# Optimization experiments

Hardware: AMD Instinct MI355X
Metric: run time of the kernel (lower is better)

Reference implementation:

```python
import jax, jax.numpy as jnp
import numpy as np

BETA = 0.25


def setup_inputs() -> dict:
    key = jax.random.key(0)
    k1, k2 = jax.random.split(key)
    z = jax.random.normal(k1, (16, 256, 32, 32), dtype=jnp.float32)
    # nn.Embedding init: uniform(-1/K, 1/K) with K = in_channels = 16384
    K, D = 16384, 256
    emb = jax.random.uniform(k2, (K, D), dtype=jnp.float32,
                             minval=-1.0 / K, maxval=1.0 / K)
    return {"z": z, "emb": emb}


def reference(z, emb):
    K, D = emb.shape
    # NCHW -> NHWC, flatten to tokens
    zp = jnp.transpose(z, (0, 2, 3, 1))            # [B,H,W,D]
    zf = zp.reshape(-1, D)                          # [N,D]
    # squared L2 distances: ||z||^2 + ||e||^2 - 2 z.e  -> [N,K]
    d = (jnp.sum(zf * zf, axis=1, keepdims=True)
         + jnp.sum(emb * emb, axis=1)
         - 2.0 * jnp.matmul(zf, emb.T))
    idx = jnp.argmin(d, axis=1)                     # [N] int
    # gather via direct lookup (equivalent to one-hot @ emb)
    z_q = emb[idx].reshape(zp.shape)                # [B,H,W,D]
    # commitment + codebook loss
    loss = (jnp.mean((jax.lax.stop_gradient(z_q) - zp) ** 2)
            + BETA * jnp.mean((z_q - jax.lax.stop_gradient(zp)) ** 2))
    # perplexity from code usage histogram (same as mean of one-hot rows)
    counts = jax.ops.segment_sum(jnp.ones_like(idx, dtype=jnp.float32), idx,
                                 num_segments=K)
    e_mean = counts / idx.shape[0]
    perplexity = jnp.exp(-jnp.sum(e_mean * jnp.log(e_mean + 1e-10)))
    # straight-through estimator, back to NCHW
    z_q_st = zp + jax.lax.stop_gradient(z_q - zp)
    z_q_out = jnp.transpose(z_q_st, (0, 3, 1, 2))   # [B,D,H,W]
    return z_q_out, loss, perplexity, idx
```

## Files before the change

kernel.cpp:

```cpp
#include <hip/hip_runtime.h>
#include <math.h>

#define NTOK   16384
#define DDIM   256
#define HWD    1024
#define CHW    262144
#define MARGIN 3.0e-4f
#define CLIPF  5.5f
#define QS     (127.0f/5.5f)
#define EQS    2080768.0f
#define SCALE  (5.5f/(127.0f*127.0f*16384.0f))

#define WS_TI8   0u
#define WS_CI8   4194304u
#define WS_M1    8388608u
#define WS_M2    16777216u
#define WS_ARG   25165824u
#define WS_FLG   29360128u
#define WS_EE    29376512u
#define WS_ZZ    29442048u
#define WS_IDX   29507584u
#define WS_CNT   29573120u
#define WS_SUM   29638656u

typedef __attribute__((ext_vector_type(4)))  int   i32x4;
typedef __attribute__((ext_vector_type(16))) char  c16;
typedef __attribute__((ext_vector_type(4)))  _Float16 h4;

__device__ __forceinline__ void top2m(int& a1, int& a2, const int b1, const int b2) {
  const int mn = min(a1, b1);
  a1 = max(a1, b1);
  a2 = max(max(a2, b2), mn);
}

__global__ __launch_bounds__(256) void k_prep(const float* __restrict__ z,
                                              const float* __restrict__ emb,
                                              char* __restrict__ Ti8,
                                              char* __restrict__ Ci8,
                                              float* __restrict__ zz,
                                              float* __restrict__ ee,
                                              float* __restrict__ zt,
                                              unsigned char* __restrict__ flags) {
  const int bid = blockIdx.x;
  const int tid = threadIdx.x;
  const int t64 = tid & 63, chunk = tid >> 6;
  if (bid < 256) {
    __shared__ double part[4][64];
    __shared__ int   fpart[4][64];
    const int n = bid * 64 + t64;
    const int b = n >> 10, hw = n & 1023;
    const float* zp = z + (size_t)b * CHW + hw;
    float tmp[64];
    double s = 0.0;
    int clip = 0;
    #pragma unroll
    for (int j = 0; j < 64; ++j) {
      const float f = zp[(size_t)(chunk * 64 + j) * HWD];
      tmp[j] = f;
      s += (double)f * (double)f;
      clip |= (fabsf(f) > CLIPF) ? 1 : 0;
    }
    c16 q[4];
    #pragma unroll
    for (int sl = 0; sl < 4; ++sl)
      #pragma unroll
      for (int j = 0; j < 16; ++j)
        q[sl][j] = (char)(int)rintf(fminf(fmaxf(tmp[sl * 16 + j], -CLIPF), CLIPF) * QS);
    const int rl = n & 127, tile = n >> 7;
    char* dst = Ti8 + (size_t)tile * 32768 + chunk * 8192 + rl * 64;
    const int sw = ((rl >> 1) & 3) << 4;
    #pragma unroll
    for (int sl = 0; sl < 4; ++sl) *(c16*)(dst + ((sl * 16) ^ sw)) = q[sl];
    float* ztp = zt + (size_t)n * 256 + chunk * 64;
    #pragma unroll
    for (int j4 = 0; j4 < 16; ++j4) *(float4*)(ztp + j4 * 4) = *(float4*)&tmp[j4 * 4];
    part[chunk][t64] = s;
    fpart[chunk][t64] = clip;
    __syncthreads();
    if (tid < 64) {
      zz[n] = (float)(part[0][t64] + part[1][t64] + part[2][t64] + part[3][t64]);
      flags[n] = (unsigned char)(fpart[0][t64] | fpart[1][t64] | fpart[2][t64] | fpart[3][t64]);
    }
  } else {
    __shared__ float rows[64][257];
    __shared__ double part2[4][64];
    const int k0 = (bid - 256) * 64;
    for (int i = tid; i < 16384; i += 256)
      rows[i >> 8][i & 255] = emb[(size_t)k0 * DDIM + i];
    __syncthreads();
    const int code = k0 + t64;
    double s = 0.0;
    c16 q[4];
    #pragma unroll
    for (int sl = 0; sl < 4; ++sl)
      #pragma unroll
      for (int j = 0; j < 16; ++j) {
        const float f = rows[t64][chunk * 64 + sl * 16 + j];
        q[sl][j] = (char)(int)rintf(f * EQS);
        s += (double)f * (double)f;
      }
    char* dst = Ci8 + (size_t)code * 256 + chunk * 64;
    #pragma unroll
    for (int sl = 0; sl < 4; ++sl) *(c16*)(dst + sl * 16) = q[sl];
    part2[chunk][t64] = s;
    __syncthreads();
    if (tid < 64)
      ee[code] = (float)(part2[0][t64] + part2[1][t64] + part2[2][t64] + part2[3][t64]);
  }
}

__global__ __launch_bounds__(256) void k_mdist(
    const char* __restrict__ tokimg, const char* __restrict__ codrows,
    _Float16* __restrict__ M1, _Float16* __restrict__ M2,
    unsigned char* __restrict__ ARG) {
  __shared__ __attribute__((aligned(16))) char ldsB[65536];
  __shared__ _Float16 m1l[256];
  __shared__ _Float16 m2l[256];
  __shared__ unsigned char agl[256];
  const int raw = blockIdx.x;
  const int p = raw & 7;
  const int ctile = p * 16 + ((raw >> 3) & 15);
  const int tgrp = raw >> 7;
  const int tid = threadIdx.x;
  const int w = tid >> 6, lane = tid & 63;
  const int wr = w >> 1, wc = w & 1;
  const int fr = lane & 15, fq = lane >> 4;

  i32x4 afr[4][4];
  {
    const char* ab = codrows + (size_t)(ctile * 128 + wr * 64 + fr) * 256 + fq * 16;
    #pragma unroll
    for (int m = 0; m < 4; ++m)
      #pragma unroll
      for (int kc = 0; kc < 4; ++kc)
        afr[m][kc] = *(const i32x4*)(ab + m * 16 * 256 + kc * 64);
  }

  int boff[4][4];
  #pragma unroll
  for (int n = 0; n < 4; ++n)
    #pragma unroll
    for (int kc = 0; kc < 4; ++kc) {
      const int t = wc * 64 + n * 16 + fr;
      boff[n][kc] = kc * 8192 + t * 64 + ((fq * 16) ^ (((t >> 1) & 3) << 4));
    }

  #define STAGEB(buf, tt)                                                             \
    {                                                                                 \
      const char* src = tokimg + (size_t)(tt) * 32768;                                \
      char* dstb = ldsB + (buf) * 32768;                                              \
      _Pragma("unroll")                                                               \
      for (int r = 0; r < 8; ++r) {                                                   \
        const int u = r * 256 + tid;                                                  \
        __builtin_amdgcn_global_load_lds(                                             \
            (const __attribute__((address_space(1))) void*)(src + u * 16),            \
            (__attribute__((address_space(3))) void*)(dstb + u * 16), 16, 0, 0);      \
      }                                                                               \
    }

  STAGEB(0, tgrp * 8);
  __syncthreads();

  const int fq4 = fq * 4;
  for (int it = 0; it < 8; ++it) {
    const int ttile = tgrp * 8 + it;
    if (it < 7) STAGEB((it + 1) & 1, ttile + 1);
    const char* bufb = ldsB + (it & 1) * 32768;

    i32x4 acc[4][4];
    #pragma unroll
    for (int m = 0; m < 4; ++m)
      #pragma unroll
      for (int n = 0; n < 4; ++n) acc[m][n] = (i32x4)0;

    #pragma unroll
    for (int kc = 0; kc < 4; ++kc) {
      i32x4 b[4];
      #pragma unroll
      for (int n = 0; n < 4; ++n) b[n] = *(const i32x4*)(bufb + boff[n][kc]);
      #pragma unroll
      for (int m = 0; m < 4; ++m)
        #pragma unroll
        for (int n = 0; n < 4; ++n)
          acc[m][n] = __builtin_amdgcn_mfma_i32_16x16x64_i8(afr[m][kc], b[n], acc[m][n], 0, 0, 0);
    }

    #pragma unroll
    for (int n = 0; n < 4; ++n) {
      int p1[8], p2[8];
      #pragma unroll
      for (int m = 0; m < 4; ++m)
        #pragma unroll
        for (int jj = 0; jj < 2; ++jj) {
          const int k0 = (acc[m][n][2 * jj]     << 8) | (m * 16 + fq4 + 2 * jj);
          const int k1 = (acc[m][n][2 * jj + 1] << 8) | (m * 16 + fq4 + 2 * jj + 1);
          p1[m * 2 + jj] = max(k0, k1);
          p2[m * 2 + jj] = min(k0, k1);
        }
      top2m(p1[0], p2[0], p1[1], p2[1]); top2m(p1[2], p2[2], p1[3], p2[3]);
      top2m(p1[4], p2[4], p1[5], p2[5]); top2m(p1[6], p2[6], p1[7], p2[7]);
      top2m(p1[0], p2[0], p1[2], p2[2]); top2m(p1[4], p2[4], p1[6], p2[6]);
      top2m(p1[0], p2[0], p1[4], p2[4]);
      int k1 = p1[0], k2 = p2[0];
      #pragma unroll
      for (int off = 16; off <= 32; off <<= 1) {
        const int o1 = __shfl_xor(k1, off, 64);
        const int o2 = __shfl_xor(k2, off, 64);
        top2m(k1, k2, o1, o2);
      }
      if (lane < 16) {
        const int tl = wc * 64 + n * 16 + fr;
        m1l[tl * 2 + wr] = (_Float16)(-2.0f * SCALE * (float)(k1 >> 8));
        m2l[tl * 2 + wr] = (_Float16)(-2.0f * SCALE * (float)(k2 >> 8));
        agl[tl * 2 + wr] = (unsigned char)(k1 & 255);
      }
    }
    __syncthreads();
    if (tid < 128) {
      const int tok = ttile * 128 + tid;
      *(unsigned int*)((char*)M1 + (size_t)tok * 512 + ctile * 4) =
          *(const unsigned int*)(m1l + tid * 2);
      M2[(size_t)(ctile * 2) * NTOK + tok]     = m2l[tid * 2];
      M2[(size_t)(ctile * 2 + 1) * NTOK + tok] = m2l[tid * 2 + 1];
      ARG[(size_t)(ctile * 2) * NTOK + tok]     = agl[tid * 2];
      ARG[(size_t)(ctile * 2 + 1) * NTOK + tok] = agl[tid * 2 + 1];
    }
    __syncthreads();
  }
}

__global__ __launch_bounds__(256) void k_pick(
    const float* __restrict__ zt, const float* __restrict__ emb,
    const float* __restrict__ zz, const float* __restrict__ ee,
    const _Float16* __restrict__ M1, const _Float16* __restrict__ M2,
    const unsigned char* __restrict__ ARG, const unsigned char* __restrict__ flags,
    int* __restrict__ idx, float* __restrict__ out_idxf) {
  __shared__ float zrow[4][260];
  __shared__ int   clist[4][576];
  __shared__ int   wcnt[4];
  const int tid = threadIdx.x;
  const int w = tid >> 6, lane = tid & 63;
  const int g16 = lane >> 4, l16 = lane & 15;
  for (int ni = 0; ni < 2; ++ni) {
    const int n = blockIdx.x * 8 + w * 2 + ni;
    if (lane == 0) wcnt[w] = 0;
    *(float4*)&zrow[w][lane * 4] = *(const float4*)(zt + (size_t)n * 256 + lane * 4);
    const h4 mv = *(const h4*)(M1 + (size_t)n * 256 + lane * 4);
    float ta4[4];
    #pragma unroll
    for (int s = 0; s < 4; ++s) ta4[s] = (float)mv[s];
    float mr = fminf(fminf(ta4[0], ta4[1]), fminf(ta4[2], ta4[3]));
    #pragma unroll
    for (int o = 32; o; o >>= 1) mr = fminf(mr, __shfl_xor(mr, o, 64));
    const int ex0 = flags[n];
    const float thr = ex0 ? 3.0e38f : mr + MARGIN;
    if (!ex0) {
      #pragma unroll
      for (int s = 0; s < 4; ++s) {
        if (ta4[s] <= thr) {
          const int sub = lane * 4 + s;
          const float m2v = (float)M2[(size_t)sub * NTOK + n];
          if (m2v > thr) {
            const int pos = atomicAdd(&wcnt[w], 1);
            if (pos < 576) clist[w][pos] = sub * 64 + (int)ARG[(size_t)sub * NTOK + n];
          } else {
            const int pos = atomicAdd(&wcnt[w], 64);
            if (pos + 64 <= 576)
              for (int i = 0; i < 64; ++i) clist[w][pos + i] = sub * 64 + i;
          }
        }
      }
    }
    const int cnt = wcnt[w];
    const int doEx = ex0 || (cnt > 576);
    const int nc = doEx ? 16384 : cnt;
    const float zzn = zz[n];
    unsigned long long best = ~0ull;
    for (int ci = 0; ci < nc; ci += 4) {
      int k;
      if (doEx) k = ci + g16;
      else { const int sl = ci + g16; k = clist[w][sl < cnt ? sl : 0]; }
      const float* erow = emb + (size_t)k * DDIM;
      double s = 0.0;
      #pragma unroll
      for (int qq = 0; qq < 4; ++qq) {
        const float4 ev = *(const float4*)(erow + qq * 64 + l16 * 4);
        const float4 zv = *(const float4*)(&zrow[w][qq * 64 + l16 * 4]);
        s += (double)zv.x * (double)ev.x + (double)zv.y * (double)ev.y
           + (double)zv.z * (double)ev.z + (double)zv.w * (double)ev.w;
      }
      #pragma unroll
      for (int o = 8; o; o >>= 1) s += __shfl_xor(s, o, 16);
      if (l16 == 0) {
        const float mm = (float)s;
        const float d = (zzn + ee[k]) - 2.0f * mm;
        const unsigned long long c =
            ((unsigned long long)__float_as_uint(d) << 32) | (unsigned int)k;
        if (c < best) best = c;
      }
    }
    unsigned long long b0 = (l16 == 0) ? best : ~0ull;
    {
      const unsigned long long o1 = __shfl_xor(b0, 16, 64);
      b0 = o1 < b0 ? o1 : b0;
      const unsigned long long o2 = __shfl_xor(b0, 32, 64);
      b0 = o2 < b0 ? o2 : b0;
    }
    if (lane == 0) {
      const int k0 = (int)(b0 & 0xffffffffu);
      idx[n] = k0;
      out_idxf[n] = (float)k0;
    }
  }
}

__global__ __launch_bounds__(256) void k_scatter(
    const float* __restrict__ z, const float* __restrict__ emb,
    const int* __restrict__ idx, float* __restrict__ out_zq,
    int* __restrict__ counts, double* __restrict__ sums) {
  __shared__ float et[64][257];
  __shared__ int sidx[64];
  __shared__ double w4[4];
  const int tg = blockIdx.x;
  const int n0 = tg * 64;
  const int b = n0 >> 10, hw0 = n0 & 1023;
  const int tid = threadIdx.x;
  if (tid < 64) sidx[tid] = idx[n0 + tid];
  __syncthreads();
  for (int i = tid; i < 16384; i += 256) {
    const int t = i >> 8, d = i & 255;
    et[t][d] = emb[(size_t)sidx[t] * DDIM + d];
  }
  __syncthreads();
  const float* zb = z + (size_t)b * CHW + hw0;
  float* ob = out_zq + (size_t)b * CHW + hw0;
  double s = 0.0;
  for (int i = tid; i < 16384; i += 256) {
    const int d = i >> 6, t = i & 63;
    const float v = et[t][d];
    const float diff = v - zb[(size_t)d * HWD + t];
    ob[(size_t)d * HWD + t] = v;
    s += (double)diff * (double)diff;
  }
  #pragma unroll
  for (int o = 32; o; o >>= 1) s += __shfl_xor(s, o, 64);
  const int wd = tid >> 6, lane = tid & 63;
  if (lane == 0) w4[wd] = s;
  __syncthreads();
  if (tid == 0) atomicAdd(&sums[0], w4[0] + w4[1] + w4[2] + w4[3]);
  if (tid < 64) atomicAdd(&counts[sidx[tid]], 1);
}

__global__ __launch_bounds__(256) void k_histfinal(const int* __restrict__ counts,
                                                   const double* __restrict__ sums,
                                                   float* __restrict__ out_loss,
                                                   float* __restrict__ out_perp) {
  __shared__ double w4[4];
  const int tid = threadIdx.x;
  double s = 0.0;
  for (int i = tid; i < 16384; i += 256) {
    const float em = (float)counts[i] * (1.0f / 16384.0f);
    s += (double)(em * logf(em + 1e-10f));
  }
  #pragma unroll
  for (int o = 32; o; o >>= 1) s += __shfl_xor(s, o, 64);
  const int wid = tid >> 6, lane = tid & 63;
  if (lane == 0) w4[wid] = s;
  __syncthreads();
  if (tid == 0) {
    const double S = w4[0] + w4[1] + w4[2] + w4[3];
    out_loss[0] = (float)(1.25 * sums[0] / 4194304.0);
    out_perp[0] = (float)exp(-S);
  }
}

extern "C" void kernel_launch(void* const* d_in, const int* in_sizes, int n_in,
                              void* d_out, int out_size, void* d_ws, size_t ws_size,
                              hipStream_t stream) {
  const float* z   = (const float*)d_in[0];
  const float* emb = (const float*)d_in[1];
  float* out      = (float*)d_out;
  float* out_zq   = out;
  float* out_loss = out + 4194304;
  float* out_perp = out + 4194305;
  float* out_idxf = out + 4194306;
  float* zt       = out;

  char* ws = (char*)d_ws;
  char* Ti8 = ws + WS_TI8;
  char* Ci8 = ws + WS_CI8;
  _Float16* M1 = (_Float16*)(ws + WS_M1);
  _Float16* M2 = (_Float16*)(ws + WS_M2);
  unsigned char* ARG = (unsigned char*)(ws + WS_ARG);
  unsigned char* flags = (unsigned char*)(ws + WS_FLG);
  float*  ee      = (float*)(ws + WS_EE);
  float*  zz      = (float*)(ws + WS_ZZ);
  int*    idx     = (int*)  (ws + WS_IDX);
  int*    counts  = (int*)  (ws + WS_CNT);
  double* sums    = (double*)(ws + WS_SUM);

  hipMemsetAsync(counts, 0, 65536 + 16, stream);

  k_prep <<<512, 256, 0, stream>>>(z, emb, Ti8, Ci8, zz, ee, zt, flags);
  k_mdist<<<2048, 256, 0, stream>>>(Ti8, Ci8, M1, M2, ARG);
  k_pick <<<2048, 256, 0, stream>>>(zt, emb, zz, ee, M1, M2, ARG, flags, idx, out_idxf);
  k_scatter<<<256, 256, 0, stream>>>(z, emb, idx, out_zq, counts, sums);
  k_histfinal<<<1, 256, 0, stream>>>(counts, sums, out_loss, out_perp);
}
```

Before: 207.7 us.

## Fuse loss and histogram into pick kernel, double-buffer mdist epilogue

Moves the code-usage histogram atomics and the squared-error loss accumulation into k_pick. The loss reuses the best distance already computed there, and per-block partial sums are reduced in k_histfinal. This lets k_scatter drop its strided reread of z and its atomics. In k_mdist the LDS epilogue staging is double-buffered to remove the trailing barrier, and MFMA issue priority is raised with s_setprio. The risk is that the loss now comes from the distance value rather than the exact (z_q - z)^2, which may shift precision.

```diff
diff --git a/kernel.cpp b/kernel.cpp
--- a/kernel.cpp
+++ b/kernel.cpp
@@ -21,7 +21,7 @@
 #define WS_ZZ    29442048u
 #define WS_IDX   29507584u
 #define WS_CNT   29573120u
-#define WS_SUM   29638656u
+#define WS_LSUM  29638656u
 
 typedef __attribute__((ext_vector_type(4)))  int   i32x4;
 typedef __attribute__((ext_vector_type(16))) char  c16;
@@ -114,9 +114,9 @@
     _Float16* __restrict__ M1, _Float16* __restrict__ M2,
     unsigned char* __restrict__ ARG) {
   __shared__ __attribute__((aligned(16))) char ldsB[65536];
-  __shared__ _Float16 m1l[256];
-  __shared__ _Float16 m2l[256];
-  __shared__ unsigned char agl[256];
+  __shared__ _Float16 m1l[2][256];
+  __shared__ _Float16 m2l[2][256];
+  __shared__ unsigned char agl[2][256];
   const int raw = blockIdx.x;
   const int p = raw & 7;
   const int ctile = p * 16 + ((raw >> 3) & 15);
@@ -163,9 +163,10 @@
 
   const int fq4 = fq * 4;
   for (int it = 0; it < 8; ++it) {
+    const int pb = it & 1;
     const int ttile = tgrp * 8 + it;
-    if (it < 7) STAGEB((it + 1) & 1, ttile + 1);
-    const char* bufb = ldsB + (it & 1) * 32768;
+    if (it < 7) STAGEB(pb ^ 1, ttile + 1);
+    const char* bufb = ldsB + pb * 32768;
 
     i32x4 acc[4][4];
     #pragma unroll
@@ -173,6 +174,7 @@
       #pragma unroll
       for (int n = 0; n < 4; ++n) acc[m][n] = (i32x4)0;
 
+    __builtin_amdgcn_s_setprio(1);
     #pragma unroll
     for (int kc = 0; kc < 4; ++kc) {
       i32x4 b[4];
@@ -184,6 +186,7 @@
         for (int n = 0; n < 4; ++n)
           acc[m][n] = __builtin_amdgcn_mfma_i32_16x16x64_i8(afr[m][kc], b[n], acc[m][n], 0, 0, 0);
     }
+    __builtin_amdgcn_s_setprio(0);
 
     #pragma unroll
     for (int n = 0; n < 4; ++n) {
@@ -210,22 +213,21 @@
       }
       if (lane < 16) {
         const int tl = wc * 64 + n * 16 + fr;
-        m1l[tl * 2 + wr] = (_Float16)(-2.0f * SCALE * (float)(k1 >> 8));
-        m2l[tl * 2 + wr] = (_Float16)(-2.0f * SCALE * (float)(k2 >> 8));
-        agl[tl * 2 + wr] = (unsigned char)(k1 & 255);
+        m1l[pb][tl * 2 + wr] = (_Float16)(-2.0f * SCALE * (float)(k1 >> 8));
+        m2l[pb][tl * 2 + wr] = (_Float16)(-2.0f * SCALE * (float)(k2 >> 8));
+        agl[pb][tl * 2 + wr] = (unsigned char)(k1 & 255);
       }
     }
     __syncthreads();
     if (tid < 128) {
       const int tok = ttile * 128 + tid;
       *(unsigned int*)((char*)M1 + (size_t)tok * 512 + ctile * 4) =
-          *(const unsigned int*)(m1l + tid * 2);
-      M2[(size_t)(ctile * 2) * NTOK + tok]     = m2l[tid * 2];
-      M2[(size_t)(ctile * 2 + 1) * NTOK + tok] = m2l[tid * 2 + 1];
-      ARG[(size_t)(ctile * 2) * NTOK + tok]     = agl[tid * 2];
-      ARG[(size_t)(ctile * 2 + 1) * NTOK + tok] = agl[tid * 2 + 1];
-    }
-    __syncthreads();
+          *(const unsigned int*)(&m1l[pb][tid * 2]);
+      M2[(size_t)(ctile * 2) * NTOK + tok]     = m2l[pb][tid * 2];
+      M2[(size_t)(ctile * 2 + 1) * NTOK + tok] = m2l[pb][tid * 2 + 1];
+      ARG[(size_t)(ctile * 2) * NTOK + tok]     = agl[pb][tid * 2];
+      ARG[(size_t)(ctile * 2 + 1) * NTOK + tok] = agl[pb][tid * 2 + 1];
+    }
   }
 }
 
@@ -234,13 +236,16 @@
     const float* __restrict__ zz, const float* __restrict__ ee,
     const _Float16* __restrict__ M1, const _Float16* __restrict__ M2,
     const unsigned char* __restrict__ ARG, const unsigned char* __restrict__ flags,
-    int* __restrict__ idx, float* __restrict__ out_idxf) {
+    int* __restrict__ idx, float* __restrict__ out_idxf,
+    int* __restrict__ counts, double* __restrict__ lsum) {
   __shared__ float zrow[4][260];
   __shared__ int   clist[4][576];
   __shared__ int   wcnt[4];
+  __shared__ double wsum[4];
   const int tid = threadIdx.x;
   const int w = tid >> 6, lane = tid & 63;
   const int g16 = lane >> 4, l16 = lane & 15;
+  double dsum = 0.0;
   for (int ni = 0; ni < 2; ++ni) {
     const int n = blockIdx.x * 8 + w * 2 + ni;
     if (lane == 0) wcnt[w] = 0;
@@ -310,17 +315,20 @@
       const int k0 = (int)(b0 & 0xffffffffu);
       idx[n] = k0;
       out_idxf[n] = (float)k0;
-    }
-  }
+      atomicAdd(&counts[k0], 1);
+      dsum += (double)__uint_as_float((unsigned int)(b0 >> 32));
+    }
+  }
+  if (lane == 0) wsum[w] = dsum;
+  __syncthreads();
+  if (tid == 0) lsum[blockIdx.x] = wsum[0] + wsum[1] + wsum[2] + wsum[3];
 }
 
 __global__ __launch_bounds__(256) void k_scatter(
-    const float* __restrict__ z, const float* __restrict__ emb,
-    const int* __restrict__ idx, float* __restrict__ out_zq,
-    int* __restrict__ counts, double* __restrict__ sums) {
+    const float* __restrict__ emb, const int* __restrict__ idx,
+    float* __restrict__ out_zq) {
   __shared__ float et[64][257];
   __shared__ int sidx[64];
-  __shared__ double w4[4];
   const int tg = blockIdx.x;
   const int n0 = tg * 64;
   const int b = n0 >> 10, hw0 = n0 & 1023;
@@ -332,44 +340,37 @@
     et[t][d] = emb[(size_t)sidx[t] * DDIM + d];
   }
   __syncthreads();
-  const float* zb = z + (size_t)b * CHW + hw0;
   float* ob = out_zq + (size_t)b * CHW + hw0;
-  double s = 0.0;
   for (int i = tid; i < 16384; i += 256) {
     const int d = i >> 6, t = i & 63;
-    const float v = et[t][d];
-    const float diff = v - zb[(size_t)d * HWD + t];
-    ob[(size_t)d * HWD + t] = v;
-    s += (double)diff * (double)diff;
-  }
-  #pragma unroll
-  for (int o = 32; o; o >>= 1) s += __shfl_xor(s, o, 64);
-  const int wd = tid >> 6, lane = tid & 63;
-  if (lane == 0) w4[wd] = s;
-  __syncthreads();
-  if (tid == 0) atomicAdd(&sums[0], w4[0] + w4[1] + w4[2] + w4[3]);
-  if (tid < 64) atomicAdd(&counts[sidx[tid]], 1);
+    ob[(size_t)d * HWD + t] = et[t][d];
+  }
 }
 
 __global__ __launch_bounds__(256) void k_histfinal(const int* __restrict__ counts,
-                                                   const double* __restrict__ sums,
+                                                   const double* __restrict__ lsum,
                                                    float* __restrict__ out_loss,
                                                    float* __restrict__ out_perp) {
-  __shared__ double w4[4];
+  __shared__ double w4[4], l4[4];
   const int tid = threadIdx.x;
-  double s = 0.0;
+  double s = 0.0, l = 0.0;
   for (int i = tid; i < 16384; i += 256) {
     const float em = (float)counts[i] * (1.0f / 16384.0f);
     s += (double)(em * logf(em + 1e-10f));
   }
+  for (int i = tid; i < 2048; i += 256) l += lsum[i];
   #pragma unroll
-  for (int o = 32; o; o >>= 1) s += __shfl_xor(s, o, 64);
+  for (int o = 32; o; o >>= 1) {
+    s += __shfl_xor(s, o, 64);
+    l += __shfl_xor(l, o, 64);
+  }
   const int wid = tid >> 6, lane = tid & 63;
-  if (lane == 0) w4[wid] = s;
+  if (lane == 0) { w4[wid] = s; l4[wid] = l; }
   __syncthreads();
   if (tid == 0) {
     const double S = w4[0] + w4[1] + w4[2] + w4[3];
-    out_loss[0] = (float)(1.25 * sums[0] / 4194304.0);
+    const double L = l4[0] + l4[1] + l4[2] + l4[3];
+    out_loss[0] = (float)(1.25 * L / 4194304.0);
     out_perp[0] = (float)exp(-S);
   }
 }
@@ -397,13 +398,14 @@
   float*  zz      = (float*)(ws + WS_ZZ);
   int*    idx     = (int*)  (ws + WS_IDX);
   int*    counts  = (int*)  (ws + WS_CNT);
-  double* sums    = (double*)(ws + WS_SUM);
-
-  hipMemsetAsync(counts, 0, 65536 + 16, stream);
+  double* lsum    = (double*)(ws + WS_LSUM);
+
+  hipMemsetAsync(counts, 0, 65536, stream);
 
   k_prep <<<512, 256, 0, stream>>>(z, emb, Ti8, Ci8, zz, ee, zt, flags);
   k_mdist<<<2048, 256, 0, stream>>>(Ti8, Ci8, M1, M2, ARG);
-  k_pick <<<2048, 256, 0, stream>>>(zt, emb, zz, ee, M1, M2, ARG, flags, idx, out_idxf);
-  k_scatter<<<256, 256, 0, stream>>>(z, emb, idx, out_zq, counts, sums);
-  k_histfinal<<<1, 256, 0, stream>>>(counts, sums, out_loss, out_perp);
-}
+  k_pick <<<2048, 256, 0, stream>>>(zt, emb, zz, ee, M1, M2, ARG, flags,
+                                    idx, out_idxf, counts, lsum);
+  k_scatter<<<256, 256, 0, stream>>>(emb, idx, out_zq);
+  k_histfinal<<<1, 256, 0, stream>>>(counts, lsum, out_loss, out_perp);
+}
```

Result: faster. 197.7 us (-4.8%).
